# Kernel optimization log

Hardware: AMD Instinct MI355X
Metric: run time of the kernel (lower is better)

Reference implementation:

```python
import jax, jax.numpy as jnp
import numpy as np

B, T, DIM = 4, 2048, 1024
H, DH = 16, 64  # num_heads, dim_head; weight_dim = H*DH = 1024
SCALE = DIM ** (-0.5)  # note: original scales by dim**-0.5, not dim_head**-0.5


def setup_inputs() -> dict:
    key = jax.random.key(0)
    k1, k2, k3 = jax.random.split(key, 3)
    x = jax.random.normal(k1, (B, T, DIM), dtype=jnp.float32)
    w_qkv = jax.random.normal(k2, (3 * H * DH, DIM), dtype=jnp.float32) * (DIM ** -0.5)
    w_out = jax.random.normal(k3, (DIM, H * DH), dtype=jnp.float32) * ((H * DH) ** -0.5)
    b_out = jnp.zeros((DIM,), dtype=jnp.float32)
    return {"x": x, "w_qkv": w_qkv, "w_out": w_out, "b_out": b_out}


def reference(x, w_qkv, w_out, b_out):
    # qkv: [b, t, 3*H*DH] (torch Linear: x @ W^T)
    qkv = jnp.einsum('btc,oc->bto', x, w_qkv)
    # rearrange 'b t (d k h) -> k b h t d' with k=3, h=H: d is the OUTERMOST
    # factor of the flattened axis, then k, then h (h fastest-varying).
    qkv = qkv.reshape(B, T, DH, 3, H)          # [b, t, d, k, h]
    qkv = jnp.transpose(qkv, (3, 0, 4, 1, 2))   # [k, b, h, t, d]
    q, k, v = qkv[0], qkv[1], qkv[2]
    # scores: [b, h, t, t]
    attn = jnp.einsum('bhid,bhjd->bhij', q, k) * SCALE
    attn = jax.nn.softmax(attn, axis=-1)
    out = jnp.einsum('bhij,bhjd->bhid', attn, v)           # [b, h, t, d]
    out = jnp.transpose(out, (0, 2, 1, 3)).reshape(B, T, H * DH)  # 'b h t d -> b t (h d)'
    return jnp.einsum('btc,oc->bto', out, w_out) + b_out
```

## Files before the change

kernel.cpp:

```cpp
#include <hip/hip_runtime.h>
#include <hip/hip_bf16.h>


typedef __attribute__((ext_vector_type(8))) short short8;
typedef __attribute__((ext_vector_type(4))) float floatx4;

static __device__ __forceinline__ floatx4 mfma16(short8 a, short8 b, floatx4 c) {
    return __builtin_amdgcn_mfma_f32_16x16x32_bf16(a, b, c, 0, 0, 0);
}

static __device__ __forceinline__ unsigned short f2bf_bits(float f) {
    __hip_bfloat16 h = __float2bfloat16(f);
    return *reinterpret_cast<unsigned short*>(&h);
}

static __device__ __forceinline__ float fast_exp2(float x) {
#if __has_builtin(__builtin_amdgcn_exp2f)
    return __builtin_amdgcn_exp2f(x);
#else
    return exp2f(x);
#endif
}

#define GLD16(gptr, ldsptr)                                                  \
    __builtin_amdgcn_global_load_lds(                                        \
        (const __attribute__((address_space(1))) void*)(gptr),               \
        (__attribute__((address_space(3))) void*)(ldsptr), 16, 0, 0)

__global__ __launch_bounds__(256) void k_cvt(
    const float* __restrict__ src, unsigned short* __restrict__ dst, int n4)
{
    typedef __attribute__((ext_vector_type(4))) unsigned short ushort4v;
    for (int i = blockIdx.x * blockDim.x + threadIdx.x; i < n4;
         i += gridDim.x * blockDim.x) {
        const float4 v = ((const float4*)src)[i];
        ushort4v o;
        o.x = f2bf_bits(v.x);
        o.y = f2bf_bits(v.y);
        o.z = f2bf_bits(v.z);
        o.w = f2bf_bits(v.w);
        ((ushort4v*)dst)[i] = o;
    }
}

__global__ __launch_bounds__(256) void k_qkv(
    const unsigned short* __restrict__ x,
    const unsigned short* __restrict__ wq,
    unsigned short* __restrict__ qb,
    unsigned short* __restrict__ kb,
    unsigned short* __restrict__ vb)
{
    __shared__ unsigned short As[128 * 32];
    __shared__ unsigned short Bs[128 * 32];

    const int tid  = threadIdx.x;
    const int wave = tid >> 6, lane = tid & 63;
    const int quad = lane >> 4, l16 = lane & 15;
    const int wm = wave >> 1, wn = wave & 1;
    const int m0 = blockIdx.y * 128;
    const int kk = blockIdx.x >> 3;
    const int d0 = (blockIdx.x & 7) * 8;
    const int kkh = kk * 16;

    const int srow = lane >> 2;
    const int sc8  = (lane & 3) * 8;
    const int row0 = wave * 32 + srow;
    const int row1 = row0 + 16;
    const int bn0  = (d0 + (row0 >> 4)) * 48 + kkh + (row0 & 15);
    const int bn1  = (d0 + (row1 >> 4)) * 48 + kkh + (row1 & 15);

    floatx4 acc[4][4];
#pragma unroll
    for (int i = 0; i < 4; i++)
#pragma unroll
        for (int j = 0; j < 4; j++) acc[i][j] = (floatx4){0.f, 0.f, 0.f, 0.f};

    for (int k0 = 0; k0 < 1024; k0 += 32) {
        GLD16(&x[(m0 + row0) * 1024 + k0 + sc8], &As[(wave * 32) * 32]);
        GLD16(&x[(m0 + row1) * 1024 + k0 + sc8], &As[(wave * 32 + 16) * 32]);
        GLD16(&wq[bn0 * 1024 + k0 + sc8],        &Bs[(wave * 32) * 32]);
        GLD16(&wq[bn1 * 1024 + k0 + sc8],        &Bs[(wave * 32 + 16) * 32]);
        __syncthreads();

        short8 af[4], bfv[4];
#pragma unroll
        for (int mi = 0; mi < 4; mi++)
            af[mi] = *(const short8*)&As[(wm * 64 + mi * 16 + l16) * 32 + quad * 8];
#pragma unroll
        for (int ni = 0; ni < 4; ni++)
            bfv[ni] = *(const short8*)&Bs[(wn * 64 + ni * 16 + l16) * 32 + quad * 8];
#pragma unroll
        for (int mi = 0; mi < 4; mi++)
#pragma unroll
            for (int ni = 0; ni < 4; ni++)
                acc[mi][ni] = mfma16(af[mi], bfv[ni], acc[mi][ni]);
        __syncthreads();
    }

    unsigned short* dst = (kk == 0) ? qb : (kk == 1) ? kb : vb;
    const float scale = (kk == 0) ? 0.045084220027780106f : 1.0f;
#pragma unroll
    for (int ni = 0; ni < 4; ni++) {
        const int d = d0 + wn * 4 + ni;
#pragma unroll
        for (int mi = 0; mi < 4; mi++) {
            const int m  = m0 + wm * 64 + mi * 16 + quad * 4;
            const int b  = m >> 11;
            const int tt = m & 2047;
            ushort4 pk;
            pk.x = f2bf_bits(acc[mi][ni][0] * scale);
            pk.y = f2bf_bits(acc[mi][ni][1] * scale);
            pk.z = f2bf_bits(acc[mi][ni][2] * scale);
            pk.w = f2bf_bits(acc[mi][ni][3] * scale);
            *(ushort4*)&dst[((b * 16 + l16) * 64 + d) * 2048 + tt] = pk;
        }
    }
}

__global__ __launch_bounds__(256) void k_tr(
    const unsigned short* __restrict__ src,
    unsigned short* __restrict__ dst)
{
    __shared__ unsigned short Ts[64 * 72];
    const int tid = threadIdx.x;
    const int bh  = blockIdx.y;
    const int t0  = blockIdx.x * 64;
    const int dg  = (tid >> 4) * 4;
    const int tg  = (tid & 15) * 4;

    ushort4 rv[4];
#pragma unroll
    for (int dd = 0; dd < 4; dd++)
        rv[dd] = *(const ushort4*)&src[(bh * 64 + dg + dd) * 2048 + t0 + tg];
#pragma unroll
    for (int tt = 0; tt < 4; tt++) {
        ushort4 wv;
        wv.x = ((const unsigned short*)&rv[0])[tt];
        wv.y = ((const unsigned short*)&rv[1])[tt];
        wv.z = ((const unsigned short*)&rv[2])[tt];
        wv.w = ((const unsigned short*)&rv[3])[tt];
        *(ushort4*)&Ts[(tg + tt) * 72 + dg] = wv;
    }
    __syncthreads();

    const int tr = tid >> 2;
    const int c8 = (tid & 3) * 8;
    *(uint4*)&dst[(bh * 2048 + t0 + tr) * 64 + c8]      = *(const uint4*)&Ts[tr * 72 + c8];
    *(uint4*)&dst[(bh * 2048 + t0 + tr) * 64 + c8 + 32] = *(const uint4*)&Ts[tr * 72 + c8 + 32];
}

__global__ __launch_bounds__(512) void k_attn(
    const unsigned short* __restrict__ qt,
    const unsigned short* __restrict__ kt,
    const unsigned short* __restrict__ vg,
    __hip_bfloat16* __restrict__ og)
{
    __shared__ unsigned short Ks[64 * 72];
    __shared__ unsigned short Vt[64 * 72];
    __shared__ unsigned short Pt[8 * 32 * 72];

    const int tid  = threadIdx.x;
    const int wave = tid >> 6, lane = tid & 63;
    const int quad = lane >> 4, l16 = lane & 15;
    const int blk = blockIdx.x;
    const int bh  = (blk & 7) | ((blk >> 6) << 3);
    const int q0  = ((blk >> 3) & 7) * 256;
    const int qr  = q0 + wave * 32;

    short8 qf[2][2];
#pragma unroll
    for (int mi = 0; mi < 2; mi++)
#pragma unroll
        for (int ks = 0; ks < 2; ks++)
            qf[mi][ks] = *(const short8*)&qt[(bh * 2048 + qr + mi * 16 + l16) * 64 + ks * 32 + quad * 8];

    float lsum[2] = {0.f, 0.f};
    floatx4 o[2][4];
#pragma unroll
    for (int mi = 0; mi < 2; mi++)
#pragma unroll
        for (int di = 0; di < 4; di++) o[mi][di] = (floatx4){0.f, 0.f, 0.f, 0.f};

    const int srow = tid >> 3;
    const int sc8  = (tid & 7) * 8;

    for (int j0 = 0; j0 < 2048; j0 += 64) {
        *(uint4*)&Ks[srow * 72 + sc8] = *(const uint4*)&kt[(bh * 2048 + j0 + srow) * 64 + sc8];
        *(uint4*)&Vt[srow * 72 + sc8] = *(const uint4*)&vg[(bh * 64 + srow) * 2048 + j0 + sc8];
        __syncthreads();

        floatx4 st[2][4];
#pragma unroll
        for (int mi = 0; mi < 2; mi++)
#pragma unroll
            for (int nk = 0; nk < 4; nk++) st[mi][nk] = (floatx4){0.f, 0.f, 0.f, 0.f};
#pragma unroll
        for (int ks = 0; ks < 2; ks++) {
            short8 kf[4];
#pragma unroll
            for (int nk = 0; nk < 4; nk++)
                kf[nk] = *(const short8*)&Ks[(nk * 16 + l16) * 72 + ks * 32 + quad * 8];
#pragma unroll
            for (int mi = 0; mi < 2; mi++)
#pragma unroll
                for (int nk = 0; nk < 4; nk++)
                    st[mi][nk] = mfma16(kf[nk], qf[mi][ks], st[mi][nk]);
        }

#pragma unroll
        for (int mi = 0; mi < 2; mi++) {
#pragma unroll
            for (int nk = 0; nk < 4; nk++) {
                const float p0 = fast_exp2(st[mi][nk][0]);
                const float p1 = fast_exp2(st[mi][nk][1]);
                const float p2 = fast_exp2(st[mi][nk][2]);
                const float p3 = fast_exp2(st[mi][nk][3]);
                lsum[mi] += (p0 + p1) + (p2 + p3);
                ushort4 pk;
                pk.x = f2bf_bits(p0);
                pk.y = f2bf_bits(p1);
                pk.z = f2bf_bits(p2);
                pk.w = f2bf_bits(p3);
                *(ushort4*)&Pt[(wave * 32 + mi * 16 + l16) * 72 + nk * 16 + quad * 4] = pk;
            }
        }
        __builtin_amdgcn_s_waitcnt(0xc07f);

#pragma unroll
        for (int ks = 0; ks < 2; ks++) {
            short8 pf[2], vf[4];
#pragma unroll
            for (int mi = 0; mi < 2; mi++)
                pf[mi] = *(const short8*)&Pt[(wave * 32 + mi * 16 + l16) * 72 + ks * 32 + quad * 8];
#pragma unroll
            for (int di = 0; di < 4; di++)
                vf[di] = *(const short8*)&Vt[(di * 16 + l16) * 72 + ks * 32 + quad * 8];
#pragma unroll
            for (int mi = 0; mi < 2; mi++)
#pragma unroll
                for (int di = 0; di < 4; di++)
                    o[mi][di] = mfma16(pf[mi], vf[di], o[mi][di]);
        }
        __syncthreads();
    }

#pragma unroll
    for (int mi = 0; mi < 2; mi++) {
        float t = lsum[mi];
        t += __shfl_xor(t, 16);
        t += __shfl_xor(t, 32);
        lsum[mi] = t;
    }

    const int b = bh >> 4, h = bh & 15;
#pragma unroll
    for (int mi = 0; mi < 2; mi++) {
#pragma unroll
        for (int r = 0; r < 4; r++) {
            const float inv = 1.0f / __shfl(lsum[mi], quad * 4 + r);
            const int t = qr + mi * 16 + quad * 4 + r;
#pragma unroll
            for (int di = 0; di < 4; di++)
                og[(b * 2048 + t) * 1024 + h * 64 + di * 16 + l16] =
                    __float2bfloat16(o[mi][di][r] * inv);
        }
    }
}

__global__ __launch_bounds__(256) void k_out(
    const unsigned short* __restrict__ a,
    const unsigned short* __restrict__ wq,
    const float* __restrict__ bias,
    float* __restrict__ out)
{
    __shared__ unsigned short As[128 * 32];
    __shared__ unsigned short Bs[128 * 32];

    const int tid  = threadIdx.x;
    const int wave = tid >> 6, lane = tid & 63;
    const int quad = lane >> 4, l16 = lane & 15;
    const int wm = wave >> 1, wn = wave & 1;
    const int m0 = blockIdx.y * 128, n0 = blockIdx.x * 128;

    const int srow = lane >> 2;
    const int sc8  = (lane & 3) * 8;
    const int row0 = wave * 32 + srow;
    const int row1 = row0 + 16;

    floatx4 acc[4][4];
#pragma unroll
    for (int i = 0; i < 4; i++)
#pragma unroll
        for (int j = 0; j < 4; j++) acc[i][j] = (floatx4){0.f, 0.f, 0.f, 0.f};

    for (int k0 = 0; k0 < 1024; k0 += 32) {
        GLD16(&a[(m0 + row0) * 1024 + k0 + sc8],  &As[(wave * 32) * 32]);
        GLD16(&a[(m0 + row1) * 1024 + k0 + sc8],  &As[(wave * 32 + 16) * 32]);
        GLD16(&wq[(n0 + row0) * 1024 + k0 + sc8], &Bs[(wave * 32) * 32]);
        GLD16(&wq[(n0 + row1) * 1024 + k0 + sc8], &Bs[(wave * 32 + 16) * 32]);
        __syncthreads();

        short8 af[4], bfv[4];
#pragma unroll
        for (int mi = 0; mi < 4; mi++)
            af[mi] = *(const short8*)&As[(wm * 64 + mi * 16 + l16) * 32 + quad * 8];
#pragma unroll
        for (int ni = 0; ni < 4; ni++)
            bfv[ni] = *(const short8*)&Bs[(wn * 64 + ni * 16 + l16) * 32 + quad * 8];
#pragma unroll
        for (int mi = 0; mi < 4; mi++)
#pragma unroll
            for (int ni = 0; ni < 4; ni++)
                acc[mi][ni] = mfma16(af[mi], bfv[ni], acc[mi][ni]);
        __syncthreads();
    }

#pragma unroll
    for (int ni = 0; ni < 4; ni++) {
        const int col = n0 + wn * 64 + ni * 16 + l16;
        const float bv = bias[col];
#pragma unroll
        for (int mi = 0; mi < 4; mi++) {
            const int mbase = m0 + wm * 64 + mi * 16 + quad * 4;
#pragma unroll
            for (int r = 0; r < 4; r++)
                out[(mbase + r) * 1024 + col] = acc[mi][ni][r] + bv;
        }
    }
}

extern "C" void kernel_launch(void* const* d_in, const int* in_sizes, int n_in,
                              void* d_out, int out_size, void* d_ws, size_t ws_size,
                              hipStream_t stream) {
    const float* x    = (const float*)d_in[0];
    const float* wqkv = (const float*)d_in[1];
    const float* wout = (const float*)d_in[2];
    const float* bout = (const float*)d_in[3];
    float* out = (float*)d_out;

    unsigned short* ws = (unsigned short*)d_ws;
    unsigned short* xb    = ws;
    unsigned short* wqkvb = xb + 8388608;
    unsigned short* woutb = wqkvb + 3145728;
    unsigned short* qb    = woutb + 1048576;
    unsigned short* kb    = qb + 8388608;
    unsigned short* vb    = kb + 8388608;
    unsigned short* ob    = vb + 8388608;

    k_cvt<<<2048, 256, 0, stream>>>(x,    xb,    8388608 / 4);
    k_cvt<<<1024, 256, 0, stream>>>(wqkv, wqkvb, 3145728 / 4);
    k_cvt<<<512,  256, 0, stream>>>(wout, woutb, 1048576 / 4);

    k_qkv<<<dim3(24, 64), 256, 0, stream>>>(xb, wqkvb, qb, kb, vb);

    k_tr<<<dim3(32, 64), 256, 0, stream>>>(qb, xb);
    k_tr<<<dim3(32, 64), 256, 0, stream>>>(kb, qb);

    k_attn<<<512, 512, 0, stream>>>(xb, qb, vb, (__hip_bfloat16*)ob);
    k_out<<<dim3(8, 64), 256, 0, stream>>>(ob, woutb, bout, out);
}
```

Measured before the change: 308.4 us.

## Load K/V fragments directly from global memory in attention, drop shared staging

The attention kernel no longer stages K and V tiles in shared memory with block-wide barriers. Each wave now loads its MFMA operand fragments for K and V straight from global memory, relying on L1/L2 for reuse. Blocks shrink to 4 waves over 128 queries and the grid doubles, removing the per-iteration __syncthreads. The trade is that every wave reissues the same global loads, so cache traffic rises, and load latency is exposed with no explicit prefetch.

```diff
diff --git a/kernel.cpp b/kernel.cpp
--- a/kernel.cpp
+++ b/kernel.cpp
@@ -149,23 +149,24 @@
     *(uint4*)&dst[(bh * 2048 + t0 + tr) * 64 + c8 + 32] = *(const uint4*)&Ts[tr * 72 + c8 + 32];
 }
 
-__global__ __launch_bounds__(512) void k_attn(
+__global__ __launch_bounds__(256) void k_attn(
     const unsigned short* __restrict__ qt,
     const unsigned short* __restrict__ kt,
     const unsigned short* __restrict__ vg,
     __hip_bfloat16* __restrict__ og)
 {
-    __shared__ unsigned short Ks[64 * 72];
-    __shared__ unsigned short Vt[64 * 72];
-    __shared__ unsigned short Pt[8 * 32 * 72];
+    __shared__ unsigned short Pt[4 * 32 * 72];
 
     const int tid  = threadIdx.x;
     const int wave = tid >> 6, lane = tid & 63;
     const int quad = lane >> 4, l16 = lane & 15;
     const int blk = blockIdx.x;
-    const int bh  = (blk & 7) | ((blk >> 6) << 3);
-    const int q0  = ((blk >> 3) & 7) * 256;
+    const int bh  = (blk & 7) | ((blk >> 7) << 3);
+    const int q0  = ((blk >> 3) & 15) * 128;
     const int qr  = q0 + wave * 32;
+
+    const unsigned short* kbase = kt + bh * 2048 * 64;
+    const unsigned short* vbase = vg + bh * 64 * 2048;
 
     short8 qf[2][2];
 #pragma unroll
@@ -181,13 +182,13 @@
 #pragma unroll
         for (int di = 0; di < 4; di++) o[mi][di] = (floatx4){0.f, 0.f, 0.f, 0.f};
 
-    const int srow = tid >> 3;
-    const int sc8  = (tid & 7) * 8;
-
     for (int j0 = 0; j0 < 2048; j0 += 64) {
-        *(uint4*)&Ks[srow * 72 + sc8] = *(const uint4*)&kt[(bh * 2048 + j0 + srow) * 64 + sc8];
-        *(uint4*)&Vt[srow * 72 + sc8] = *(const uint4*)&vg[(bh * 64 + srow) * 2048 + j0 + sc8];
-        __syncthreads();
+        short8 kf[2][4];
+#pragma unroll
+        for (int ks = 0; ks < 2; ks++)
+#pragma unroll
+            for (int nk = 0; nk < 4; nk++)
+                kf[ks][nk] = *(const short8*)&kbase[(j0 + nk * 16 + l16) * 64 + ks * 32 + quad * 8];
 
         floatx4 st[2][4];
 #pragma unroll
@@ -195,17 +196,12 @@
 #pragma unroll
             for (int nk = 0; nk < 4; nk++) st[mi][nk] = (floatx4){0.f, 0.f, 0.f, 0.f};
 #pragma unroll
-        for (int ks = 0; ks < 2; ks++) {
-            short8 kf[4];
-#pragma unroll
-            for (int nk = 0; nk < 4; nk++)
-                kf[nk] = *(const short8*)&Ks[(nk * 16 + l16) * 72 + ks * 32 + quad * 8];
+        for (int ks = 0; ks < 2; ks++)
 #pragma unroll
             for (int mi = 0; mi < 2; mi++)
 #pragma unroll
                 for (int nk = 0; nk < 4; nk++)
-                    st[mi][nk] = mfma16(kf[nk], qf[mi][ks], st[mi][nk]);
-        }
+                    st[mi][nk] = mfma16(kf[ks][nk], qf[mi][ks], st[mi][nk]);
 
 #pragma unroll
         for (int mi = 0; mi < 2; mi++) {
@@ -224,24 +220,30 @@
                 *(ushort4*)&Pt[(wave * 32 + mi * 16 + l16) * 72 + nk * 16 + quad * 4] = pk;
             }
         }
+
+        short8 vf[2][4];
+#pragma unroll
+        for (int ks = 0; ks < 2; ks++)
+#pragma unroll
+            for (int di = 0; di < 4; di++)
+                vf[ks][di] = *(const short8*)&vbase[(di * 16 + l16) * 2048 + j0 + ks * 32 + quad * 8];
+
         __builtin_amdgcn_s_waitcnt(0xc07f);
 
-#pragma unroll
-        for (int ks = 0; ks < 2; ks++) {
-            short8 pf[2], vf[4];
+        short8 pf[2][2];
+#pragma unroll
+        for (int ks = 0; ks < 2; ks++)
 #pragma unroll
             for (int mi = 0; mi < 2; mi++)
-                pf[mi] = *(const short8*)&Pt[(wave * 32 + mi * 16 + l16) * 72 + ks * 32 + quad * 8];
-#pragma unroll
-            for (int di = 0; di < 4; di++)
-                vf[di] = *(const short8*)&Vt[(di * 16 + l16) * 72 + ks * 32 + quad * 8];
+                pf[ks][mi] = *(const short8*)&Pt[(wave * 32 + mi * 16 + l16) * 72 + ks * 32 + quad * 8];
+
+#pragma unroll
+        for (int ks = 0; ks < 2; ks++)
 #pragma unroll
             for (int mi = 0; mi < 2; mi++)
 #pragma unroll
                 for (int di = 0; di < 4; di++)
-                    o[mi][di] = mfma16(pf[mi], vf[di], o[mi][di]);
-        }
-        __syncthreads();
+                    o[mi][di] = mfma16(pf[ks][mi], vf[ks][di], o[mi][di]);
     }
 
 #pragma unroll
@@ -356,6 +358,6 @@
     k_tr<<<dim3(32, 64), 256, 0, stream>>>(qb, xb);
     k_tr<<<dim3(32, 64), 256, 0, stream>>>(kb, qb);
 
-    k_attn<<<512, 512, 0, stream>>>(xb, qb, vb, (__hip_bfloat16*)ob);
+    k_attn<<<1024, 256, 0, stream>>>(xb, qb, vb, (__hip_bfloat16*)ob);
     k_out<<<dim3(8, 64), 256, 0, stream>>>(ob, woutb, bout, out);
 }
```

After: 480.9 us. +55.9%, slower.
